# Kernel tuning notes

Hardware: AMD Instinct MI355X
Metric: run time of the kernel (lower is better)

## Reference

```python
import jax, jax.numpy as jnp
import numpy as np

B, S, H, OUT, STEPS = 64, 1024, 512, 256, 32


def setup_inputs() -> dict:
    key = jax.random.key(0)
    ks = jax.random.split(key, 10)
    s = 0.02
    return {
        "encoder_outputs": jax.random.normal(ks[0], (B, S, H), jnp.float32),
        "hidden": jax.random.normal(ks[1], (B, H), jnp.float32),
        # Attention: nn.Linear(2H, 1)
        "attn_w": jax.random.normal(ks[2], (2 * H,), jnp.float32) * s,
        "attn_b": jax.random.normal(ks[3], (1,), jnp.float32) * s,
        # LSTMCell(OUT + H, H): torch gate order i, f, g, o
        "w_ih": jax.random.normal(ks[4], (4 * H, OUT + H), jnp.float32) * s,
        "w_hh": jax.random.normal(ks[5], (4 * H, H), jnp.float32) * s,
        "b_ih": jax.random.normal(ks[6], (4 * H,), jnp.float32) * s,
        "b_hh": jax.random.normal(ks[7], (4 * H,), jnp.float32) * s,
        # fc: nn.Linear(H, OUT)
        "fc_w": jax.random.normal(ks[8], (OUT, H), jnp.float32) * s,
        "fc_b": jax.random.normal(ks[9], (OUT,), jnp.float32) * s,
    }


def reference(encoder_outputs, hidden, attn_w, attn_b, w_ih, w_hh, b_ih, b_hh, fc_w, fc_b):
    # Split attention weight: Linear(concat(enc, hid)) == enc@wa_e + hid@wa_d + b
    wa_e, wa_d = attn_w[:H], attn_w[H:]
    # encoder contribution to attention energy is step-invariant: [B, S]
    enc_energy = jnp.einsum("bsh,h->bs", encoder_outputs, wa_e) + attn_b[0]
    bias = b_ih + b_hh  # [4H]

    def step(carry, _):
        h, c, dec_in = carry
        # Bahdanau-style energy and context
        energy = enc_energy + (h @ wa_d)[:, None]          # [B, S]
        weights = jax.nn.softmax(energy, axis=1)
        context = jnp.einsum("bs,bsh->bh", weights, encoder_outputs)
        # LSTMCell (torch gate order i, f, g, o)
        x = jnp.concatenate([dec_in, context], axis=1)     # [B, OUT+H]
        gates = x @ w_ih.T + h @ w_hh.T + bias             # [B, 4H]
        i, f, g, o = jnp.split(gates, 4, axis=1)
        c_new = jax.nn.sigmoid(f) * c + jax.nn.sigmoid(i) * jnp.tanh(g)
        h_new = jax.nn.sigmoid(o) * jnp.tanh(c_new)
        dec_new = h_new @ fc_w.T + fc_b                    # [B, OUT]
        return (h_new, c_new, dec_new), dec_new

    dec0 = jnp.zeros((encoder_outputs.shape[0], fc_w.shape[0]), encoder_outputs.dtype)
    c0 = jnp.zeros_like(hidden)
    _, outs = jax.lax.scan(step, (hidden, c0, dec0), None, length=STEPS)
    return jnp.transpose(outs, (1, 0, 2))  # [B, STEPS, OUT]
```

## Files before the change

kernel.cpp:

```cpp
#include <hip/hip_runtime.h>
#include <math.h>

#define B 64
#define S 1024
#define H 512
#define OUT 256
#define STEPS 32
#define NG 2048
#define X 768

typedef __attribute__((ext_vector_type(8))) short short8;
typedef __attribute__((ext_vector_type(4))) short s16x4;
typedef __attribute__((ext_vector_type(4))) float f32x4;
typedef __attribute__((ext_vector_type(4))) unsigned u32x4;

__device__ __forceinline__ float sigf(float x) { return 1.0f / (1.0f + __expf(-x)); }
__device__ __forceinline__ float tanhf_fast(float x) {
  return 2.0f / (1.0f + __expf(-2.0f * x)) - 1.0f;
}

__device__ __forceinline__ short f2bf(float x) {
  union { float f; unsigned u; } a; a.f = x;
  unsigned r = a.u + 0x7fffu + ((a.u >> 16) & 1u);
  return (short)(r >> 16);
}
__device__ __forceinline__ float bf2f(short s) {
  union { unsigned u; float f; } a; a.u = ((unsigned)(unsigned short)s) << 16;
  return a.f;
}

__device__ __forceinline__ unsigned load_u32_cg(const unsigned* p) {
  unsigned r;
  asm volatile("global_load_dword %0, %1, off sc0 sc1\n\ts_waitcnt vmcnt(0)"
               : "=v"(r) : "v"(p) : "memory");
  return r;
}

__global__ __launch_bounds__(256) void k_pre(
    const float* __restrict__ enc, const float* __restrict__ attn_w,
    float* __restrict__ part_ctx, float* __restrict__ part_ml,
    const float* __restrict__ w_ih, const float* __restrict__ w_hh,
    const float* __restrict__ fc_w, short* __restrict__ whi,
    short* __restrict__ wlo) {
  __shared__ float smem[6208];
  const int cid = blockIdx.x;
  const int tid = threadIdx.x;
  if (cid < 2048) {
    float* sm_acc = smem;
    float* sm_l = smem + 2048;
    const int b = cid >> 5, chunk = cid & 31;
    const int wave = tid >> 6, lane = tid & 63;
    const float4 wa0 = *(const float4*)(attn_w + lane * 8);
    const float4 wa1 = *(const float4*)(attn_w + lane * 8 + 4);
    const float* eb = enc + (long)b * S * H + (long)(chunk * 32 + wave) * H + lane * 8;
    float4 v0[8], v1[8];
#pragma unroll
    for (int i = 0; i < 8; ++i) {
      const float* row = eb + (long)i * 4 * H;
      v0[i] = *(const float4*)row;
      v1[i] = *(const float4*)(row + 4);
    }
    float l = 0.0f;
    float acc[8];
#pragma unroll
    for (int r = 0; r < 8; ++r) acc[r] = 0.0f;
#pragma unroll
    for (int i = 0; i < 8; ++i) {
      float e = v0[i].x * wa0.x + v0[i].y * wa0.y + v0[i].z * wa0.z + v0[i].w * wa0.w +
                v1[i].x * wa1.x + v1[i].y * wa1.y + v1[i].z * wa1.z + v1[i].w * wa1.w;
#pragma unroll
      for (int msk = 1; msk < 64; msk <<= 1) e += __shfl_xor(e, msk, 64);
      const float p = __expf(e);
      l += p;
      acc[0] = fmaf(p, v0[i].x, acc[0]); acc[1] = fmaf(p, v0[i].y, acc[1]);
      acc[2] = fmaf(p, v0[i].z, acc[2]); acc[3] = fmaf(p, v0[i].w, acc[3]);
      acc[4] = fmaf(p, v1[i].x, acc[4]); acc[5] = fmaf(p, v1[i].y, acc[5]);
      acc[6] = fmaf(p, v1[i].z, acc[6]); acc[7] = fmaf(p, v1[i].w, acc[7]);
    }
#pragma unroll
    for (int r = 0; r < 8; ++r) sm_acc[wave * 512 + lane * 8 + r] = acc[r];
    if (lane == 0) sm_l[wave] = l;
    __syncthreads();
    const int h0 = tid * 2;
    float s0 = 0.f, s1 = 0.f;
#pragma unroll
    for (int w = 0; w < 4; ++w) {
      s0 += sm_acc[w * 512 + h0];
      s1 += sm_acc[w * 512 + h0 + 1];
    }
    float* pc = part_ctx + ((long)chunk * B + b) * H;
    pc[h0] = s0; pc[h0 + 1] = s1;
    if (tid == 0)
      part_ml[chunk * B + b] = sm_l[0] + sm_l[1] + sm_l[2] + sm_l[3];
  } else {
    float* ft = smem;
    float* wd = smem + 4128;
    const int n0 = (cid - 2048) * 8;
    for (int i = tid; i < 512; i += 256) {
      const int r = i >> 6, c4 = (i & 63) << 2;
      *(float4*)&wd[r * 260 + c4] = *(const float4*)(w_ih + (long)(n0 + r) * X + c4);
    }
    float acc[16];
#pragma unroll
    for (int e = 0; e < 16; ++e) acc[e] = 0.f;
    const int n_l = tid >> 5, kq = tid & 31;
    for (int jt = 0; jt < 32; ++jt) {
      __syncthreads();
      for (int i = tid; i < 1024; i += 256) {
        const int r = i >> 7, c4 = (i & 127) << 2;
        *(float4*)&ft[r * 516 + c4] =
            *(const float4*)(fc_w + (long)(jt * 8 + r) * H + c4);
      }
      __syncthreads();
#pragma unroll 2
      for (int j = 0; j < 8; ++j) {
        const float w = wd[n_l * 260 + jt * 8 + j];
#pragma unroll
        for (int e4 = 0; e4 < 4; ++e4) {
          const float4 f = *(float4*)&ft[j * 516 + kq * 4 + e4 * 128];
          acc[e4 * 4 + 0] = fmaf(w, f.x, acc[e4 * 4 + 0]);
          acc[e4 * 4 + 1] = fmaf(w, f.y, acc[e4 * 4 + 1]);
          acc[e4 * 4 + 2] = fmaf(w, f.z, acc[e4 * 4 + 2]);
          acc[e4 * 4 + 3] = fmaf(w, f.w, acc[e4 * 4 + 3]);
        }
      }
    }
    const long rbase = (long)(n0 + n_l) * H;
#pragma unroll
    for (int e4 = 0; e4 < 4; ++e4) {
      const int k = kq * 4 + e4 * 128;
      const float4 hh = *(const float4*)(w_hh + rbase + k);
      float v[4] = {acc[e4 * 4] + hh.x, acc[e4 * 4 + 1] + hh.y,
                    acc[e4 * 4 + 2] + hh.z, acc[e4 * 4 + 3] + hh.w};
      s16x4 hi4, lo4;
#pragma unroll
      for (int e = 0; e < 4; ++e) {
        const short hb = f2bf(v[e]);
        hi4[e] = hb;
        lo4[e] = f2bf(v[e] - bf2f(hb));
      }
      *(s16x4*)(whi + rbase + k) = hi4;
      *(s16x4*)(wlo + rbase + k) = lo4;
    }
  }
}

__global__ __launch_bounds__(256) void k_ctx_sum(
    const float* __restrict__ part_ctx, const float* __restrict__ part_ml,
    float* __restrict__ ctx) {
  const int b = blockIdx.x;
  float L = 0.f;
#pragma unroll
  for (int c = 0; c < 32; ++c) L += part_ml[c * B + b];
  const float inv = 1.0f / L;
  const int h0 = threadIdx.x * 2;
  float s0 = 0.f, s1 = 0.f;
#pragma unroll
  for (int c = 0; c < 32; ++c) {
    const float* pc = part_ctx + ((long)c * B + b) * H;
    s0 += pc[h0]; s1 += pc[h0 + 1];
  }
  ctx[(long)b * H + h0] = s0 * inv;
  ctx[(long)b * H + h0 + 1] = s1 * inv;
}

__global__ __launch_bounds__(256) void k_gbase(
    const float* __restrict__ w_ih, const float* __restrict__ w_hh,
    const float* __restrict__ b_ih, const float* __restrict__ b_hh,
    const float* __restrict__ fc_b, const float* __restrict__ ctx,
    const float* __restrict__ hidden, float* __restrict__ gates0,
    float* __restrict__ gbase2) {
  __shared__ float wt[128][33];
  __shared__ float rb[16][524];
  __shared__ float sfc[256];
  const int n0 = blockIdx.x * 32, b0 = blockIdx.y * 16;
  const int tid = threadIdx.x;
  const int n_l = tid & 31, bh = tid >> 5;
  const int n = n0 + n_l;

  sfc[tid] = fc_b[tid];
  for (int i = tid; i < 16 * 128; i += 256) {
    const int r = i >> 7, c4 = (i & 127) << 2;
    *(float4*)&rb[r][c4] = *(const float4*)(ctx + (long)(b0 + r) * H + c4);
  }

  float a1a = 0.f, a1b = 0.f;
  for (int kc = 0; kc < 4; ++kc) {
    __syncthreads();
    for (int i = tid; i < 4096; i += 256) {
      const int r = i >> 7, c = i & 127;
      wt[c][r] = w_ih[(long)(n0 + r) * X + OUT + kc * 128 + c];
    }
    __syncthreads();
#pragma unroll 8
    for (int k = 0; k < 128; ++k) {
      const float wv = wt[k][n_l];
      a1a = fmaf(wv, rb[bh][kc * 128 + k], a1a);
      a1b = fmaf(wv, rb[bh + 8][kc * 128 + k], a1b);
    }
  }

  float db = 0.f;
  for (int kc = 0; kc < 2; ++kc) {
    __syncthreads();
    for (int i = tid; i < 4096; i += 256) {
      const int r = i >> 7, c = i & 127;
      wt[c][r] = w_ih[(long)(n0 + r) * X + kc * 128 + c];
    }
    __syncthreads();
#pragma unroll 8
    for (int k = 0; k < 128; ++k) db = fmaf(wt[k][n_l], sfc[kc * 128 + k], db);
  }

  __syncthreads();
  for (int i = tid; i < 16 * 128; i += 256) {
    const int r = i >> 7, c = (i & 127) << 2;
    *(float4*)&rb[r][c] = *(const float4*)(hidden + (long)(b0 + r) * H + c);
  }
  float a2a = 0.f, a2b = 0.f;
  for (int kc = 0; kc < 4; ++kc) {
    __syncthreads();
    for (int i = tid; i < 4096; i += 256) {
      const int r = i >> 7, c = i & 127;
      wt[c][r] = w_hh[(long)(n0 + r) * H + kc * 128 + c];
    }
    __syncthreads();
#pragma unroll 8
    for (int k = 0; k < 128; ++k) {
      const float wv = wt[k][n_l];
      a2a = fmaf(wv, rb[bh][kc * 128 + k], a2a);
      a2b = fmaf(wv, rb[bh + 8][kc * 128 + k], a2b);
    }
  }

  const float bias = b_ih[n] + b_hh[n];
  gates0[(long)(b0 + bh) * NG + n]     = a1a + bias + a2a;
  gates0[(long)(b0 + bh + 8) * NG + n] = a1b + bias + a2b;
  gbase2[(long)(b0 + bh) * NG + n]     = a1a + bias + db;
  gbase2[(long)(b0 + bh + 8) * NG + n] = a1b + bias + db;
}

#define HSTR 520
__global__ __launch_bounds__(256, 1) void k_recur3(
    const short* __restrict__ whi, const short* __restrict__ wlo,
    const float* __restrict__ gb2, const float* __restrict__ gates0,
    unsigned* __restrict__ hsbf, unsigned int* __restrict__ bar) {
  __shared__ short sh_hi[16 * HSTR];
  __shared__ short sh_lo[16 * HSTR];
  __shared__ float sG[4][8][20];
  __shared__ float sgb[8][64];
  __shared__ float scell[8][16];
  __shared__ int s_fast;

  const int blk = blockIdx.x;
  const int bg = blk & 7;
  const int slice = blk >> 3;
  const int b8 = bg << 3;
  const int hc0 = slice << 4;
  const int tid = threadIdx.x;
  const int w = tid >> 6, l = tid & 63;
  const int ln = l & 15, lk = l >> 4;

  if (tid == 0) {
    unsigned xcc;
    asm volatile("s_getreg_b32 %0, hwreg(20, 0, 32)" : "=s"(xcc));
    __hip_atomic_fetch_or(&bar[7936 + bg], 1u << (xcc & 0xFu),
                          __ATOMIC_RELEASE, __HIP_MEMORY_SCOPE_AGENT);
    unsigned* gbar = &bar[7944 + bg];
    __hip_atomic_fetch_add(gbar, 1u, __ATOMIC_RELEASE, __HIP_MEMORY_SCOPE_AGENT);
    while (load_u32_cg(gbar) < 32u) __builtin_amdgcn_s_sleep(1);
    const unsigned mask = __hip_atomic_load(&bar[7936 + bg], __ATOMIC_ACQUIRE,
                                            __HIP_MEMORY_SCOPE_AGENT);
    s_fast = (__popc(mask) == 1) ? 1 : 0;
  }
  __syncthreads();
  const bool fast = (s_fast != 0);

  for (int i = tid; i < 16 * HSTR; i += 256) { sh_hi[i] = 0; sh_lo[i] = 0; }

  for (int idx = tid; idx < 512; idx += 256) {
    const int b = idx >> 6, gr = idx & 63, g = gr >> 4, j = gr & 15;
    sgb[b][gr] = gb2[(long)(b8 + b) * NG + (g << 9) + hc0 + j];
  }

  short8 wh[16], wl[16];
  {
    const long wb = (long)((w << 9) + hc0 + ln) * H + (lk << 3);
#pragma unroll
    for (int kk = 0; kk < 16; ++kk) {
      wh[kk] = *(const short8*)(whi + wb + kk * 32);
      wl[kk] = *(const short8*)(wlo + wb + kk * 32);
    }
  }
  __syncthreads();

  if (tid < 128) {
    const int b = tid >> 4, j = tid & 15;
    const float* g0 = gates0 + (long)(b8 + b) * NG + hc0 + j;
    const float gi = g0[0];
    const float gg = g0[1024];
    const float go = g0[1536];
    const float cn = sigf(gi) * tanhf_fast(gg);
    const float hn = sigf(go) * tanhf_fast(cn);
    scell[b][j] = cn;
    const short hi = f2bf(hn);
    const short lo = f2bf(hn - bf2f(hi));
    hsbf[(long)(b8 + b) * H + hc0 + j] =
        (unsigned)(unsigned short)hi | ((unsigned)(unsigned short)lo << 16);
    asm volatile("s_waitcnt vmcnt(0)" ::: "memory");
  }
  __syncthreads();
  if (tid == 0) {
    unsigned* f0 = bar + bg * 32;
    if (fast)
      __hip_atomic_fetch_add(&f0[slice], 1u, __ATOMIC_RELAXED, __HIP_MEMORY_SCOPE_AGENT);
    else
      __hip_atomic_fetch_add(&f0[slice], 1u, __ATOMIC_RELEASE, __HIP_MEMORY_SCOPE_AGENT);
  }

  for (int t = 1; t < STEPS; ++t) {
    unsigned* flags = bar + (t - 1) * 256 + bg * 32;
    const unsigned* hb = hsbf + (long)(t - 1) * B * H + (long)b8 * H;
    if (fast) {
      const unsigned* fl = flags + (w << 3);
      while (!__all(load_u32_cg(fl + (l & 7)) != 0u)) {}
      const int colu = (w << 7) + ((l & 31) << 2);
      const int r0 = (l >> 5) << 2;
#pragma unroll
      for (int q = 0; q < 4; ++q) {
        const int row = r0 + q;
        const u32x4 v = *(const u32x4*)(hb + (long)row * H + colu);
        s16x4 hi4, lo4;
#pragma unroll
        for (int e = 0; e < 4; ++e) {
          hi4[e] = (short)(v[e] & 0xFFFFu);
          lo4[e] = (short)(v[e] >> 16);
        }
        *(s16x4*)&sh_hi[row * HSTR + colu] = hi4;
        *(s16x4*)&sh_lo[row * HSTR + colu] = lo4;
      }
    } else {
      if (tid < 64) {
        while (!__all(load_u32_cg(flags + (tid & 31)) != 0u)) {}
      }
      if (tid == 0)
        (void)__hip_atomic_load(&flags[0], __ATOMIC_ACQUIRE, __HIP_MEMORY_SCOPE_AGENT);
      __syncthreads();
#pragma unroll
      for (int q = 0; q < 4; ++q) {
        const int d0 = q * 1024 + tid * 4;
        const u32x4 v = *(const u32x4*)(hb + d0);
        const int row = d0 >> 9, col = d0 & 511;
        s16x4 hi4, lo4;
#pragma unroll
        for (int e = 0; e < 4; ++e) {
          hi4[e] = (short)(v[e] & 0xFFFFu);
          lo4[e] = (short)(v[e] >> 16);
        }
        *(s16x4*)&sh_hi[row * HSTR + col] = hi4;
        *(s16x4*)&sh_lo[row * HSTR + col] = lo4;
      }
    }
    __syncthreads();

    f32x4 a0 = {0.f, 0.f, 0.f, 0.f};
    f32x4 a1 = {0.f, 0.f, 0.f, 0.f};
    f32x4 a2 = {0.f, 0.f, 0.f, 0.f};
    asm volatile("s_nop 3" ::);
    const int abase = ln * HSTR + (lk << 3);
#pragma unroll
    for (int kk = 0; kk < 16; ++kk) {
      const short8 ah = *(const short8*)&sh_hi[abase + kk * 32];
      const short8 al = *(const short8*)&sh_lo[abase + kk * 32];
      asm volatile("v_mfma_f32_16x16x32_bf16 %0, %1, %2, %0"
                   : "+v"(a0) : "v"(ah), "a"(wh[kk]));
      asm volatile("v_mfma_f32_16x16x32_bf16 %0, %1, %2, %0"
                   : "+v"(a1) : "v"(al), "a"(wh[kk]));
      asm volatile("v_mfma_f32_16x16x32_bf16 %0, %1, %2, %0"
                   : "+v"(a2) : "v"(ah), "a"(wl[kk]));
    }
    asm volatile("s_nop 7\n\ts_nop 7" ::);
    if (lk < 2) {
#pragma unroll
      for (int r = 0; r < 4; ++r)
        sG[w][(lk << 2) + r][ln] = a0[r] + a1[r] + a2[r];
    }
    __syncthreads();

    if (tid < 128) {
      const int b = tid >> 4, j = tid & 15;
      const float gi = sG[0][b][j] + sgb[b][j];
      const float gf = sG[1][b][j] + sgb[b][16 + j];
      const float gg = sG[2][b][j] + sgb[b][32 + j];
      const float go = sG[3][b][j] + sgb[b][48 + j];
      const float c_old = scell[b][j];
      const float cn = sigf(gf) * c_old + sigf(gi) * tanhf_fast(gg);
      const float hn = sigf(go) * tanhf_fast(cn);
      scell[b][j] = cn;
      const short hi = f2bf(hn);
      const short lo = f2bf(hn - bf2f(hi));
      hsbf[(long)t * B * H + (long)(b8 + b) * H + hc0 + j] =
          (unsigned)(unsigned short)hi | ((unsigned)(unsigned short)lo << 16);
      asm volatile("s_waitcnt vmcnt(0)" ::: "memory");
    }
    __syncthreads();

    if (t < STEPS - 1) {
      if (tid == 0) {
        unsigned* nf = bar + t * 256 + bg * 32;
        if (fast)
          __hip_atomic_fetch_add(&nf[slice], 1u, __ATOMIC_RELAXED,
                                 __HIP_MEMORY_SCOPE_AGENT);
        else
          __hip_atomic_fetch_add(&nf[slice], 1u, __ATOMIC_RELEASE,
                                 __HIP_MEMORY_SCOPE_AGENT);
      }
    }
  }
}

__global__ __launch_bounds__(256) void k_dec2(
    const unsigned* __restrict__ hsbf, const float* __restrict__ fc_w,
    const float* __restrict__ fc_b, float* __restrict__ out) {
  __shared__ float A[32 * 68];
  __shared__ float Bm[64 * 68];
  const int m0 = blockIdx.x * 32;
  const int o0 = blockIdx.y * 64;
  const int tid = threadIdx.x;
  const int tn = tid & 15, tm = tid >> 4;
  float acc[2][4] = {{0.f, 0.f, 0.f, 0.f}, {0.f, 0.f, 0.f, 0.f}};
  for (int k0 = 0; k0 < H; k0 += 64) {
    for (int idx = tid; idx < 512; idx += 256) {
      const int r = idx >> 4, k4 = idx & 15;
      const u32x4 v = *(const u32x4*)&hsbf[(long)(m0 + r) * H + k0 + k4 * 4];
#pragma unroll
      for (int e = 0; e < 4; ++e)
        A[r * 68 + k4 * 4 + e] =
            bf2f((short)(v[e] & 0xFFFFu)) + bf2f((short)(v[e] >> 16));
    }
    for (int idx = tid; idx < 1024; idx += 256) {
      const int r = idx >> 4, k4 = idx & 15;
      *(float4*)&Bm[r * 68 + k4 * 4] =
          *(const float4*)&fc_w[(long)(o0 + r) * H + k0 + k4 * 4];
    }
    __syncthreads();
#pragma unroll
    for (int k4 = 0; k4 < 16; ++k4) {
      const float4 a0 = *(float4*)&A[tm * 68 + k4 * 4];
      const float4 a1 = *(float4*)&A[(tm + 16) * 68 + k4 * 4];
      const float4 b0 = *(float4*)&Bm[tn * 68 + k4 * 4];
      const float4 b1 = *(float4*)&Bm[(tn + 16) * 68 + k4 * 4];
      const float4 b2 = *(float4*)&Bm[(tn + 32) * 68 + k4 * 4];
      const float4 b3 = *(float4*)&Bm[(tn + 48) * 68 + k4 * 4];
      acc[0][0] += a0.x * b0.x + a0.y * b0.y + a0.z * b0.z + a0.w * b0.w;
      acc[0][1] += a0.x * b1.x + a0.y * b1.y + a0.z * b1.z + a0.w * b1.w;
      acc[0][2] += a0.x * b2.x + a0.y * b2.y + a0.z * b2.z + a0.w * b2.w;
      acc[0][3] += a0.x * b3.x + a0.y * b3.y + a0.z * b3.z + a0.w * b3.w;
      acc[1][0] += a1.x * b0.x + a1.y * b0.y + a1.z * b0.z + a1.w * b0.w;
      acc[1][1] += a1.x * b1.x + a1.y * b1.y + a1.z * b1.z + a1.w * b1.w;
      acc[1][2] += a1.x * b2.x + a1.y * b2.y + a1.z * b2.z + a1.w * b2.w;
      acc[1][3] += a1.x * b3.x + a1.y * b3.y + a1.z * b3.z + a1.w * b3.w;
    }
    __syncthreads();
  }
#pragma unroll
  for (int i = 0; i < 2; ++i) {
    const int m = m0 + tm + 16 * i;
    const int t = m >> 6, b = m & 63;
#pragma unroll
    for (int j = 0; j < 4; ++j) {
      const int o = o0 + tn + 16 * j;
      out[((long)b * STEPS + t) * OUT + o] = acc[i][j] + fc_b[o];
    }
  }
}

extern "C" void kernel_launch(void* const* d_in, const int* in_sizes, int n_in,
                              void* d_out, int out_size, void* d_ws, size_t ws_size,
                              hipStream_t stream) {
  const float* enc = (const float*)d_in[0];
  const float* hidden = (const float*)d_in[1];
  const float* attn_w = (const float*)d_in[2];
  const float* w_ih = (const float*)d_in[4];
  const float* w_hh = (const float*)d_in[5];
  const float* b_ih = (const float*)d_in[6];
  const float* b_hh = (const float*)d_in[7];
  const float* fc_w = (const float*)d_in[8];
  const float* fc_b = (const float*)d_in[9];
  float* out = (float*)d_out;

  float* ws = (float*)d_ws;
  short* whi      = (short*)ws;
  short* wlo      = whi + 1048576;
  float* gates0   = (float*)(wlo + 1048576);
  float* gbase2   = gates0 + 131072;
  unsigned* hsbf  = (unsigned*)(gbase2 + 131072);
  float* part_ctx = (float*)hsbf;
  float* part_ml  = (float*)(hsbf + 1048576);
  float* ctx      = part_ml + 2048;
  unsigned int* bar = (unsigned int*)(ctx + 32768);

  hipMemsetAsync(bar, 0, 7952 * sizeof(unsigned int), stream);
  k_pre<<<2304, 256, 0, stream>>>(enc, attn_w, part_ctx, part_ml,
                                  w_ih, w_hh, fc_w, whi, wlo);
  k_ctx_sum<<<64, 256, 0, stream>>>(part_ctx, part_ml, ctx);
  k_gbase<<<dim3(64, 4), 256, 0, stream>>>(w_ih, w_hh, b_ih, b_hh, fc_b, ctx,
                                           hidden, gates0, gbase2);

  k_recur3<<<256, 256, 0, stream>>>(whi, wlo, gbase2, gates0, hsbf, bar);

  k_dec2<<<dim3(64, 4), 256, 0, stream>>>(hsbf, fc_w, fc_b, out);
}
```

Baseline: 263.8 us.

## Split fused precompute into separate context and weight-fold kernels with fewer chunks

Separates the merged precompute kernel into a context-partials kernel and a weight-folding kernel launched back to back. The context kernel now gives each block 128 sequence rows in 8 groups of 16, computes energies through a shared-memory reduction instead of wave shuffles, and re-reads the encoder rows to accumulate the weighted context. This cuts the partial count from 32 to 8 per batch row, so the final sum does less work. In exchange, the two jobs no longer overlap in one launch, the encoder is read twice, and the loop adds extra barriers.

```diff
diff --git a/kernel.cpp b/kernel.cpp
--- a/kernel.cpp
+++ b/kernel.cpp
@@ -36,112 +36,112 @@
   return r;
 }
 
-__global__ __launch_bounds__(256) void k_pre(
+__global__ __launch_bounds__(256) void k_ctx(
     const float* __restrict__ enc, const float* __restrict__ attn_w,
-    float* __restrict__ part_ctx, float* __restrict__ part_ml,
+    float* __restrict__ part_ctx, float* __restrict__ part_ml) {
+  __shared__ float part[16][65];
+  __shared__ float sp[128];
+  const int tid = threadIdx.x;
+  const int b = blockIdx.x >> 3, chunk = blockIdx.x & 7;
+  const int wave = tid >> 6, lane = tid & 63;
+  const float4 wa0 = *(const float4*)(attn_w + lane * 8);
+  const float4 wa1 = *(const float4*)(attn_w + lane * 8 + 4);
+  const float* eb = enc + (long)b * S * H + (long)(chunk * 128) * H;
+  const int h0 = tid * 2;
+  float s0 = 0.f, s1 = 0.f;
+  for (int g = 0; g < 8; ++g) {
+#pragma unroll
+    for (int i = 0; i < 4; ++i) {
+      const int rl = wave * 4 + i;
+      const float* r = eb + (long)(g * 16 + rl) * H + lane * 8;
+      const float4 v0 = *(const float4*)r;
+      const float4 v1 = *(const float4*)(r + 4);
+      part[rl][lane] =
+          v0.x * wa0.x + v0.y * wa0.y + v0.z * wa0.z + v0.w * wa0.w +
+          v1.x * wa1.x + v1.y * wa1.y + v1.z * wa1.z + v1.w * wa1.w;
+    }
+    __syncthreads();
+    if (tid < 16) {
+      float e = 0.f;
+#pragma unroll
+      for (int j = 0; j < 64; ++j) e += part[tid][j];
+      sp[g * 16 + tid] = __expf(e);
+    }
+    __syncthreads();
+#pragma unroll
+    for (int i = 0; i < 16; ++i) {
+      const int row = g * 16 + i;
+      const float2 v = *(const float2*)(eb + (long)row * H + h0);
+      const float p = sp[row];
+      s0 = fmaf(p, v.x, s0);
+      s1 = fmaf(p, v.y, s1);
+    }
+  }
+  float* pc = part_ctx + ((long)chunk * B + b) * H;
+  pc[h0] = s0;
+  pc[h0 + 1] = s1;
+  __syncthreads();
+  if (tid < 64) {
+    float t = sp[tid] + sp[tid + 64];
+#pragma unroll
+    for (int m = 1; m < 64; m <<= 1) t += __shfl_xor(t, m, 64);
+    if (tid == 0) part_ml[chunk * B + b] = t;
+  }
+}
+
+__global__ __launch_bounds__(256) void k_weff(
     const float* __restrict__ w_ih, const float* __restrict__ w_hh,
     const float* __restrict__ fc_w, short* __restrict__ whi,
     short* __restrict__ wlo) {
-  __shared__ float smem[6208];
-  const int cid = blockIdx.x;
+  __shared__ float ft[8 * 516];
+  __shared__ float wd[8 * 260];
   const int tid = threadIdx.x;
-  if (cid < 2048) {
-    float* sm_acc = smem;
-    float* sm_l = smem + 2048;
-    const int b = cid >> 5, chunk = cid & 31;
-    const int wave = tid >> 6, lane = tid & 63;
-    const float4 wa0 = *(const float4*)(attn_w + lane * 8);
-    const float4 wa1 = *(const float4*)(attn_w + lane * 8 + 4);
-    const float* eb = enc + (long)b * S * H + (long)(chunk * 32 + wave) * H + lane * 8;
-    float4 v0[8], v1[8];
-#pragma unroll
-    for (int i = 0; i < 8; ++i) {
-      const float* row = eb + (long)i * 4 * H;
-      v0[i] = *(const float4*)row;
-      v1[i] = *(const float4*)(row + 4);
-    }
-    float l = 0.0f;
-    float acc[8];
-#pragma unroll
-    for (int r = 0; r < 8; ++r) acc[r] = 0.0f;
-#pragma unroll
-    for (int i = 0; i < 8; ++i) {
-      float e = v0[i].x * wa0.x + v0[i].y * wa0.y + v0[i].z * wa0.z + v0[i].w * wa0.w +
-                v1[i].x * wa1.x + v1[i].y * wa1.y + v1[i].z * wa1.z + v1[i].w * wa1.w;
-#pragma unroll
-      for (int msk = 1; msk < 64; msk <<= 1) e += __shfl_xor(e, msk, 64);
-      const float p = __expf(e);
-      l += p;
-      acc[0] = fmaf(p, v0[i].x, acc[0]); acc[1] = fmaf(p, v0[i].y, acc[1]);
-      acc[2] = fmaf(p, v0[i].z, acc[2]); acc[3] = fmaf(p, v0[i].w, acc[3]);
-      acc[4] = fmaf(p, v1[i].x, acc[4]); acc[5] = fmaf(p, v1[i].y, acc[5]);
-      acc[6] = fmaf(p, v1[i].z, acc[6]); acc[7] = fmaf(p, v1[i].w, acc[7]);
-    }
-#pragma unroll
-    for (int r = 0; r < 8; ++r) sm_acc[wave * 512 + lane * 8 + r] = acc[r];
-    if (lane == 0) sm_l[wave] = l;
-    __syncthreads();
-    const int h0 = tid * 2;
-    float s0 = 0.f, s1 = 0.f;
-#pragma unroll
-    for (int w = 0; w < 4; ++w) {
-      s0 += sm_acc[w * 512 + h0];
-      s1 += sm_acc[w * 512 + h0 + 1];
-    }
-    float* pc = part_ctx + ((long)chunk * B + b) * H;
-    pc[h0] = s0; pc[h0 + 1] = s1;
-    if (tid == 0)
-      part_ml[chunk * B + b] = sm_l[0] + sm_l[1] + sm_l[2] + sm_l[3];
-  } else {
-    float* ft = smem;
-    float* wd = smem + 4128;
-    const int n0 = (cid - 2048) * 8;
-    for (int i = tid; i < 512; i += 256) {
-      const int r = i >> 6, c4 = (i & 63) << 2;
-      *(float4*)&wd[r * 260 + c4] = *(const float4*)(w_ih + (long)(n0 + r) * X + c4);
-    }
-    float acc[16];
-#pragma unroll
-    for (int e = 0; e < 16; ++e) acc[e] = 0.f;
-    const int n_l = tid >> 5, kq = tid & 31;
-    for (int jt = 0; jt < 32; ++jt) {
-      __syncthreads();
-      for (int i = tid; i < 1024; i += 256) {
-        const int r = i >> 7, c4 = (i & 127) << 2;
-        *(float4*)&ft[r * 516 + c4] =
-            *(const float4*)(fc_w + (long)(jt * 8 + r) * H + c4);
+  const int n0 = blockIdx.x * 8;
+  for (int i = tid; i < 512; i += 256) {
+    const int r = i >> 6, c4 = (i & 63) << 2;
+    *(float4*)&wd[r * 260 + c4] = *(const float4*)(w_ih + (long)(n0 + r) * X + c4);
+  }
+  float acc[16];
+#pragma unroll
+  for (int e = 0; e < 16; ++e) acc[e] = 0.f;
+  const int n_l = tid >> 5, kq = tid & 31;
+  for (int jt = 0; jt < 32; ++jt) {
+    __syncthreads();
+    for (int i = tid; i < 1024; i += 256) {
+      const int r = i >> 7, c4 = (i & 127) << 2;
+      *(float4*)&ft[r * 516 + c4] =
+          *(const float4*)(fc_w + (long)(jt * 8 + r) * H + c4);
+    }
+    __syncthreads();
+#pragma unroll 2
+    for (int j = 0; j < 8; ++j) {
+      const float w = wd[n_l * 260 + jt * 8 + j];
+#pragma unroll
+      for (int e4 = 0; e4 < 4; ++e4) {
+        const float4 f = *(float4*)&ft[j * 516 + kq * 4 + e4 * 128];
+        acc[e4 * 4 + 0] = fmaf(w, f.x, acc[e4 * 4 + 0]);
+        acc[e4 * 4 + 1] = fmaf(w, f.y, acc[e4 * 4 + 1]);
+        acc[e4 * 4 + 2] = fmaf(w, f.z, acc[e4 * 4 + 2]);
+        acc[e4 * 4 + 3] = fmaf(w, f.w, acc[e4 * 4 + 3]);
       }
-      __syncthreads();
-#pragma unroll 2
-      for (int j = 0; j < 8; ++j) {
-        const float w = wd[n_l * 260 + jt * 8 + j];
-#pragma unroll
-        for (int e4 = 0; e4 < 4; ++e4) {
-          const float4 f = *(float4*)&ft[j * 516 + kq * 4 + e4 * 128];
-          acc[e4 * 4 + 0] = fmaf(w, f.x, acc[e4 * 4 + 0]);
-          acc[e4 * 4 + 1] = fmaf(w, f.y, acc[e4 * 4 + 1]);
-          acc[e4 * 4 + 2] = fmaf(w, f.z, acc[e4 * 4 + 2]);
-          acc[e4 * 4 + 3] = fmaf(w, f.w, acc[e4 * 4 + 3]);
-        }
-      }
-    }
-    const long rbase = (long)(n0 + n_l) * H;
-#pragma unroll
-    for (int e4 = 0; e4 < 4; ++e4) {
-      const int k = kq * 4 + e4 * 128;
-      const float4 hh = *(const float4*)(w_hh + rbase + k);
-      float v[4] = {acc[e4 * 4] + hh.x, acc[e4 * 4 + 1] + hh.y,
-                    acc[e4 * 4 + 2] + hh.z, acc[e4 * 4 + 3] + hh.w};
-      s16x4 hi4, lo4;
-#pragma unroll
-      for (int e = 0; e < 4; ++e) {
-        const short hb = f2bf(v[e]);
-        hi4[e] = hb;
-        lo4[e] = f2bf(v[e] - bf2f(hb));
-      }
-      *(s16x4*)(whi + rbase + k) = hi4;
-      *(s16x4*)(wlo + rbase + k) = lo4;
-    }
+    }
+  }
+  const long rbase = (long)(n0 + n_l) * H;
+#pragma unroll
+  for (int e4 = 0; e4 < 4; ++e4) {
+    const int k = kq * 4 + e4 * 128;
+    const float4 hh = *(const float4*)(w_hh + rbase + k);
+    float v[4] = {acc[e4 * 4] + hh.x, acc[e4 * 4 + 1] + hh.y,
+                  acc[e4 * 4 + 2] + hh.z, acc[e4 * 4 + 3] + hh.w};
+    s16x4 hi4, lo4;
+#pragma unroll
+    for (int e = 0; e < 4; ++e) {
+      const short hb = f2bf(v[e]);
+      hi4[e] = hb;
+      lo4[e] = f2bf(v[e] - bf2f(hb));
+    }
+    *(s16x4*)(whi + rbase + k) = hi4;
+    *(s16x4*)(wlo + rbase + k) = lo4;
   }
 }
 
@@ -151,12 +151,12 @@
   const int b = blockIdx.x;
   float L = 0.f;
 #pragma unroll
-  for (int c = 0; c < 32; ++c) L += part_ml[c * B + b];
+  for (int c = 0; c < 8; ++c) L += part_ml[c * B + b];
   const float inv = 1.0f / L;
   const int h0 = threadIdx.x * 2;
   float s0 = 0.f, s1 = 0.f;
 #pragma unroll
-  for (int c = 0; c < 32; ++c) {
+  for (int c = 0; c < 8; ++c) {
     const float* pc = part_ctx + ((long)c * B + b) * H;
     s0 += pc[h0]; s1 += pc[h0 + 1];
   }
@@ -497,12 +497,12 @@
   unsigned* hsbf  = (unsigned*)(gbase2 + 131072);
   float* part_ctx = (float*)hsbf;
   float* part_ml  = (float*)(hsbf + 1048576);
-  float* ctx      = part_ml + 2048;
+  float* ctx      = part_ml + 512;
   unsigned int* bar = (unsigned int*)(ctx + 32768);
 
   hipMemsetAsync(bar, 0, 7952 * sizeof(unsigned int), stream);
-  k_pre<<<2304, 256, 0, stream>>>(enc, attn_w, part_ctx, part_ml,
-                                  w_ih, w_hh, fc_w, whi, wlo);
+  k_ctx<<<512, 256, 0, stream>>>(enc, attn_w, part_ctx, part_ml);
+  k_weff<<<256, 256, 0, stream>>>(w_ih, w_hh, fc_w, whi, wlo);
   k_ctx_sum<<<64, 256, 0, stream>>>(part_ctx, part_ml, ctx);
   k_gbase<<<dim3(64, 4), 256, 0, stream>>>(w_ih, w_hh, b_ih, b_hh, fc_b, ctx,
                                            hidden, gates0, gbase2);
```

After: 262.5 us. No clear change (-0.5%).
